# Kernel optimization log

Hardware: AMD Instinct MI355X
Metric: run time of the kernel (lower is better)

Reference implementation:

```python
import jax, jax.numpy as jnp
import numpy as np
import math

D = 768; H = 12; DH = 64; LAT = 512; B = 2; L = 1024


def _rms(x, w, eps=1e-6):
    return w * x * jax.lax.rsqrt(jnp.mean(x * x, axis=-1, keepdims=True) + eps)


def _rope_tables(seq_len, dh):
    inv = 1.0 / (10000.0 ** (np.arange(0, dh, 2, dtype=np.float32) / dh))
    t = np.arange(seq_len, dtype=np.float32)
    f = np.outer(t, inv)
    emb = np.concatenate([f, f], axis=-1)
    return jnp.asarray(np.cos(emb))[None, :, None, :], jnp.asarray(np.sin(emb))[None, :, None, :]


def _rope(x, cos, sin):
    x1, x2 = jnp.split(x, 2, axis=-1)
    return x * cos + jnp.concatenate([-x2, x1], axis=-1) * sin


def setup_inputs():
    key = jax.random.key(0)
    ks = jax.random.split(key, 8)
    s = 0.02
    return {
        'x': jax.random.normal(ks[0], (B, L, D), jnp.float32),
        'w_ln': jnp.ones((D,), jnp.float32),
        'w_compress': jax.random.normal(ks[1], (D, LAT), jnp.float32) * s,
        'w_qkv': jax.random.normal(ks[2], (LAT, 3 * D), jnp.float32) * s,
        'w_reso': jax.random.normal(ks[3], (LAT, H * 4), jnp.float32) * s,
        'w_qn': jnp.ones((DH,), jnp.float32),
        'w_kn': jnp.ones((DH,), jnp.float32),
        'head_decay': jnp.linspace(-3.0, 1.0, H).astype(jnp.float32),
        'temperature': jnp.ones((1,), jnp.float32) * 0.5,
        'w_out_gate': jax.random.normal(ks[4], (LAT, D), jnp.float32) * s,
        'w_proj': jax.random.normal(ks[5], (D, D), jnp.float32) * s,
        'w_memnorm': jnp.ones((D,), jnp.float32),
    }


def reference(x, w_ln, w_compress, w_qkv, w_reso, w_qn, w_kn, head_decay, temperature, w_out_gate, w_proj, w_memnorm):
    cos, sin = _rope_tables(L, DH)
    xn = _rms(x, w_ln)
    latent = jax.nn.silu(xn @ w_compress)                        # (B,L,LAT)
    q, k, v = jnp.split(latent @ w_qkv, 3, axis=-1)
    q = _rope(_rms(q.reshape(B, L, H, DH), w_qn), cos, sin)
    k = _rope(_rms(k.reshape(B, L, H, DH), w_kn), cos, sin)
    v_f = v.reshape(B, L, H, DH)
    q_f = jax.nn.elu(q) + 1.0
    k_f = jax.nn.elu(k) + 1.0
    params = (latent @ w_reso).reshape(B, L, H, 4)
    sem_amp, sem_phase, ctx_amp, ctx_phase = [params[..., i] for i in range(4)]
    sem_phase = jax.nn.sigmoid(sem_phase) * math.pi
    ctx_phase = jax.nn.sigmoid(ctx_phase) * math.pi
    decay = jnp.clip(0.3 + 0.65 * jax.nn.sigmoid(head_decay), 1e-5, 0.999)   # (H,)
    gate = jnp.clip(jax.nn.sigmoid(jax.nn.sigmoid(sem_amp) * jax.nn.sigmoid(ctx_amp)
                                   * jnp.cos(sem_phase - ctx_phase) * temperature[0]) * 1.2 - 0.1,
                    0.05, 0.95)                                  # (B,L,H)
    one_m = (1.0 - decay)[None, None, :]                          # (1,1,H)
    kv_in = jnp.einsum('blhd,blhe->blhde', k_f, v_f) * gate[..., None, None] * one_m[..., None, None]
    z_in = k_f * one_m[..., None]
    # cumulative log-decay -> df, same as torch cumsum of constant per-step log_decay
    cum_log = jnp.arange(1, L + 1, dtype=jnp.float32)[:, None] * jnp.log(decay)[None, :]
    df = jnp.exp(cum_log)[None, :, :, None]                       # (1,L,H,1)
    kv_states = jnp.cumsum(kv_in / (df[..., None] + 1e-8), axis=1) * df[..., None]
    z_states = jnp.cumsum(z_in / (df + 1e-8), axis=1) * df
    out_num = jnp.einsum('blhd,blhde->blhe', q_f, kv_states)
    den = jnp.clip(jnp.sum(q_f * z_states, axis=-1, keepdims=True), 1e-5, None)
    out = (out_num / den).reshape(B, L, D)
    return (_rms(out, w_memnorm) @ w_proj) * jax.nn.silu(latent @ w_out_gate)
```

## Files before the change

kernel.cpp:

```cpp
#include <hip/hip_runtime.h>
#include <hip/hip_bf16.h>
#include <math.h>

#define D_MODEL 768
#define NHEAD   12
#define LATD    512
#define BATCH   2
#define SEQ     1024
#define NROWS   (BATCH*SEQ)
#define NCHUNK  (SEQ/64)
#define NBH     (BATCH*NHEAD)
#define NFUSE   3200
#define PQ      72

using short8 = __attribute__((ext_vector_type(8))) short;
using f32x4  = __attribute__((ext_vector_type(4))) float;

__device__ __forceinline__ float sigf(float x){ return 1.f/(1.f+expf(-x)); }
__device__ __forceinline__ float decay_of(float hd){
  float d = 0.3f + 0.65f*sigf(hd);
  return fminf(fmaxf(d, 1e-5f), 0.999f);
}
__device__ __forceinline__ unsigned short f2b(float f){
  __hip_bfloat16 h = __float2bfloat16(f);
  return *reinterpret_cast<unsigned short*>(&h);
}
__device__ __forceinline__ float bf2f(unsigned short u){
  unsigned int x = ((unsigned int)u) << 16;
  return __uint_as_float(x);
}
__device__ __forceinline__ void async16(const unsigned short* g, unsigned short* l){
  __builtin_amdgcn_global_load_lds((const __attribute__((address_space(1))) void*)g,
                                   (__attribute__((address_space(3))) void*)l, 16, 0, 0);
}

__device__ __forceinline__ void rms_row(const float* __restrict__ xr,
    const float* __restrict__ w, unsigned short* __restrict__ yr,
    int tid, float* red)
{
  float v0 = xr[tid], v1 = xr[tid+256], v2 = xr[tid+512];
  float s = v0*v0 + v1*v1 + v2*v2;
  #pragma unroll
  for (int off=32; off; off>>=1) s += __shfl_xor(s, off, 64);
  if ((tid & 63) == 0) red[tid>>6] = s;
  __syncthreads();
  s = red[0]+red[1]+red[2]+red[3];
  float sc = rsqrtf(s*(1.f/(float)D_MODEL) + 1e-6f);
  yr[tid]     = f2b(v0*sc*w[tid]);
  yr[tid+256] = f2b(v1*sc*w[tid+256]);
  yr[tid+512] = f2b(v2*sc*w[tid+512]);
}

__global__ __launch_bounds__(256) void k_rmsnorm_bf(const float* __restrict__ x,
    const float* __restrict__ w, unsigned short* __restrict__ y)
{
  __shared__ float red[4];
  int row = blockIdx.x, tid = threadIdx.x;
  rms_row(x + (size_t)row*D_MODEL, w, y + (size_t)row*D_MODEL, tid, red);
}

__global__ __launch_bounds__(256) void k_prep(
    const float* __restrict__ x, const float* __restrict__ w_ln,
    unsigned short* __restrict__ xn,
    const float* __restrict__ wc, const float* __restrict__ wq,
    const float* __restrict__ wr, const float* __restrict__ wg,
    const float* __restrict__ wp,
    unsigned short* __restrict__ wtc, unsigned short* __restrict__ wtq,
    unsigned short* __restrict__ wtg, unsigned short* __restrict__ wtp)
{
  __shared__ unsigned short tile[64][65];
  __shared__ float red[4];
  int blk = blockIdx.x, t = threadIdx.x;
  if (blk >= 640){
    int row = blk - 640;
    rms_row(x + (size_t)row*D_MODEL, w_ln, xn + (size_t)row*D_MODEL, t, red);
    return;
  }
  const float* W; unsigned short* WT; int K, N, bx, by;
  if (blk < 96){ W=wc; WT=wtc; K=768; N=512; bx=blk&7; by=blk>>3; }
  else if (blk < 384){ int i=blk-96;  W=wq; WT=wtq; K=512; N=2304; bx=i%36; by=i/36; }
  else if (blk < 480){ int i=blk-384; W=wg; WT=wtg; K=512; N=768;  bx=i%12; by=i/12; }
  else if (blk < 624){ int i=blk-480; W=wp; WT=wtp; K=768; N=768;  bx=i%12; by=i/12; }
  else {
    int i = blk - 624;
    #pragma unroll
    for (int j=0;j<16;j++){
      int e = i*4096 + t + j*256;
      int n = 2304 + (e >> 9), k = e & 511;
      float v = (n < 2352) ? wr[(size_t)k*48 + (n-2304)] : 0.f;
      wtq[(size_t)n*512 + k] = f2b(v);
    }
    return;
  }
  int k0 = by*64, n0 = bx*64, cr = t >> 6, cc = t & 63;
  #pragma unroll
  for (int i=0;i<16;i++){
    int r = cr + i*4;
    tile[r][cc] = f2b(W[(size_t)(k0+r)*N + n0 + cc]);
  }
  __syncthreads();
  #pragma unroll
  for (int i=0;i<16;i++){
    int nn = cr + i*4;
    WT[(size_t)(n0+nn)*K + k0 + cc] = tile[cc][nn];
  }
}

__global__ __launch_bounds__(256) void k_gemm64(const unsigned short* __restrict__ A,
    const unsigned short* __restrict__ BT, float* __restrict__ Cf,
    unsigned short* __restrict__ Cb, const unsigned short* __restrict__ auxb,
    int M, int N, int K, int act, int NX)
{
  __shared__ unsigned short As[2*64*64];
  __shared__ unsigned short Bs[2*64*64];
  int tid = threadIdx.x;
  int w = tid >> 6, lane = tid & 63;
  int m16 = lane & 15, quad = lane >> 4;
  int bid = blockIdx.x, cpx = gridDim.x >> 3;
  int swz = (bid & 7)*cpx + (bid >> 3);
  int bx = swz % NX, by = swz / NX;
  int bm = by*64, bn = bx*64;

  f32x4 acc[4];
  #pragma unroll
  for (int nt=0;nt<4;nt++) acc[nt] = (f32x4){0.f,0.f,0.f,0.f};

  int nk = K >> 6;
  #pragma unroll
  for (int i=0;i<2;i++){
    int g = (w*2 + i)*64 + lane;
    int m = g >> 3, c = (g & 7) ^ (m & 7);
    async16(A  + (size_t)(bm+m)*K + c*8, As + (w*2+i)*512);
    async16(BT + (size_t)(bn+m)*K + c*8, Bs + (w*2+i)*512);
  }
  __syncthreads();
  int cur = 0;
  for (int t = 0; t < nk; ++t){
    if (t+1 < nk){
      int kk = (t+1) << 6;
      int nb = cur ^ 1;
      #pragma unroll
      for (int i=0;i<2;i++){
        int g = (w*2 + i)*64 + lane;
        int m = g >> 3, c = (g & 7) ^ (m & 7);
        async16(A  + (size_t)(bm+m)*K + kk + c*8, As + nb*4096 + (w*2+i)*512);
        async16(BT + (size_t)(bn+m)*K + kk + c*8, Bs + nb*4096 + (w*2+i)*512);
      }
    }
    #pragma unroll
    for (int s=0;s<2;s++){
      int row = w*16 + m16;
      short8 af = *(const short8*)(As + cur*4096 + (row*8 + ((s*4 + quad) ^ (row & 7)))*8);
      #pragma unroll
      for (int nt=0;nt<4;nt++){
        int n = nt*16 + m16;
        short8 bf = *(const short8*)(Bs + cur*4096 + (n*8 + ((s*4 + quad) ^ (n & 7)))*8);
        acc[nt] = __builtin_amdgcn_mfma_f32_16x16x32_bf16(af, bf, acc[nt], 0, 0, 0);
      }
    }
    __syncthreads();
    cur ^= 1;
  }
  #pragma unroll
  for (int r=0;r<4;r++){
    int row = bm + w*16 + quad*4 + r;
    #pragma unroll
    for (int nt=0;nt<4;nt++){
      int col = bn + nt*16 + m16;
      float v = acc[nt][r];
      if (act == 1) v = v/(1.f + __expf(-v));
      else if (act == 2) v *= bf2f(auxb[(size_t)row*N + col]);
      if (Cf) Cf[(size_t)row*N + col] = v;
      if (Cb) Cb[(size_t)row*N + col] = f2b(v);
    }
  }
}

__global__ __launch_bounds__(256) void k_gemm_fused(const unsigned short* __restrict__ A,
    const unsigned short* __restrict__ BT, const float* __restrict__ w_qn,
    const float* __restrict__ w_kn, const float* __restrict__ hdec,
    const float* __restrict__ temp, unsigned short* __restrict__ qf,
    unsigned short* __restrict__ kf, unsigned short* __restrict__ vf,
    float* __restrict__ cKV, float* __restrict__ cG,
    unsigned short* __restrict__ gateb)
{
  __shared__ __align__(16) unsigned short SM[4*128*64];
  unsigned short* As = SM;
  unsigned short* Bs = SM + 2*128*64;
  const int K = LATD;
  int tid = threadIdx.x;
  int w = tid >> 6, lane = tid & 63;
  int wm = (w >> 1)*64, wn = (w & 1)*64;
  int m16 = lane & 15, quad = lane >> 4;
  int bid = blockIdx.x;
  int swz = (bid & 7)*50 + (bid >> 3);
  int bx = swz >> 4, by = swz & 15;
  int bm = by*128, bn = bx*128;

  f32x4 acc[4][4];
  #pragma unroll
  for (int i=0;i<4;i++)
    #pragma unroll
    for (int j=0;j<4;j++) acc[i][j] = (f32x4){0.f,0.f,0.f,0.f};

  const int nk = K >> 6;
  #pragma unroll
  for (int i=0;i<4;i++){
    int g = (w*4 + i)*64 + lane;
    int m = g >> 3, c = (g & 7) ^ (m & 7);
    async16(A  + (size_t)(bm+m)*K + c*8, As + (w*4+i)*512);
    async16(BT + (size_t)(bn+m)*K + c*8, Bs + (w*4+i)*512);
  }
  __syncthreads();
  int cur = 0;
  for (int t = 0; t < nk; ++t){
    if (t+1 < nk){
      int kk = (t+1) << 6;
      int nb = cur ^ 1;
      #pragma unroll
      for (int i=0;i<4;i++){
        int g = (w*4 + i)*64 + lane;
        int m = g >> 3, c = (g & 7) ^ (m & 7);
        async16(A  + (size_t)(bm+m)*K + kk + c*8, As + nb*8192 + (w*4+i)*512);
        async16(BT + (size_t)(bn+m)*K + kk + c*8, Bs + nb*8192 + (w*4+i)*512);
      }
    }
    #pragma unroll
    for (int s=0;s<2;s++){
      short8 af[4], bf[4];
      #pragma unroll
      for (int mt=0;mt<4;mt++){
        int m = wm + mt*16 + m16;
        int idx = m*8 + ((s*4 + quad) ^ (m & 7));
        af[mt] = *(const short8*)(As + cur*8192 + idx*8);
      }
      #pragma unroll
      for (int nt=0;nt<4;nt++){
        int n = wn + nt*16 + m16;
        int idx = n*8 + ((s*4 + quad) ^ (n & 7));
        bf[nt] = *(const short8*)(Bs + cur*8192 + idx*8);
      }
      #pragma unroll
      for (int mt=0;mt<4;mt++)
        #pragma unroll
        for (int nt=0;nt<4;nt++)
          acc[mt][nt] = __builtin_amdgcn_mfma_f32_16x16x32_bf16(af[mt], bf[nt], acc[mt][nt], 0, 0, 0);
    }
    __syncthreads();
    cur ^= 1;
  }

  int colbase = bn + wn;
  if (colbase < 2304){
    int sec = colbase >= 1536 ? 2 : (colbase >= 768 ? 1 : 0);
    int h = (colbase - sec*768) >> 6;
    if (sec == 2){
      #pragma unroll
      for (int mt=0;mt<4;mt++)
        #pragma unroll
        for (int r=0;r<4;r++){
          int row = bm + wm + mt*16 + quad*4 + r;
          int b = row >> 10, t = row & 1023;
          size_t ob = (((size_t)(b*NHEAD+h))*SEQ + t)*64;
          #pragma unroll
          for (int nt=0;nt<4;nt++)
            vf[ob + nt*16 + m16] = f2b(acc[mt][nt][r]);
        }
    } else {
      const float* wnp = sec ? w_kn : w_qn;
      unsigned short* of = sec ? kf : qf;
      float wv4[4];
      #pragma unroll
      for (int nt=0;nt<4;nt++) wv4[nt] = wnp[nt*16 + m16];
      float inv0 = exp2f(-(float)m16*(1.f/32.f)*13.28771237954945f);
      float inv1 = inv0 * 0.01f;
      #pragma unroll
      for (int mt=0;mt<4;mt++)
        #pragma unroll
        for (int r=0;r<4;r++){
          int row = bm + wm + mt*16 + quad*4 + r;
          int b = row >> 10, t = row & 1023;
          float s = 0.f;
          #pragma unroll
          for (int nt=0;nt<4;nt++) s += acc[mt][nt][r]*acc[mt][nt][r];
          s += __shfl_xor(s, 1, 64); s += __shfl_xor(s, 2, 64);
          s += __shfl_xor(s, 4, 64); s += __shfl_xor(s, 8, 64);
          float rs = rsqrtf(s*(1.f/64.f) + 1e-6f);
          float qv[4];
          #pragma unroll
          for (int nt=0;nt<4;nt++) qv[nt] = acc[mt][nt][r]*rs*wv4[nt];
          float s0,c0,s1,c1;
          __sincosf((float)t*inv0, &s0, &c0);
          __sincosf((float)t*inv1, &s1, &c1);
          size_t ob = (((size_t)(b*NHEAD+h))*SEQ + t)*64;
          #pragma unroll
          for (int nt=0;nt<4;nt++){
            float rot = (nt < 2) ? -qv[nt+2] : qv[nt-2];
            float cs = (nt & 1) ? c1 : c0, sn = (nt & 1) ? s1 : s0;
            float val = qv[nt]*cs + rot*sn;
            val = (val > 0.f) ? val + 1.f : __expf(val);
            of[ob + nt*16 + m16] = f2b(val);
          }
        }
    }
  } else if (colbase < 2432){
    float* pf = (float*)SM;
    if (colbase == 2304){
      #pragma unroll
      for (int mt=0;mt<4;mt++)
        #pragma unroll
        for (int r=0;r<4;r++){
          int rowl = wm + mt*16 + quad*4 + r;
          #pragma unroll
          for (int nt=0;nt<4;nt++){
            int p = nt*16 + m16;
            if (p < 48) pf[rowl*49 + p] = acc[mt][nt][r];
          }
        }
    }
    __syncthreads();
    float tv = temp[0];
    #pragma unroll
    for (int i=0;i<6;i++){
      int idx2 = tid + i*256;
      int rowl = idx2 / 12, h = idx2 - rowl*12;
      int row = bm + rowl, b = row >> 10, t = row & 1023;
      const float* pr = pf + rowl*49 + h*4;
      float sa = sigf(pr[0]);
      float sp = sigf(pr[1])*3.14159265358979323846f;
      float ca = sigf(pr[2]);
      float cp = sigf(pr[3])*3.14159265358979323846f;
      float z = sa*ca*cosf(sp - cp)*tv;
      float gate = fminf(fmaxf(sigf(z)*1.2f - 0.1f, 0.05f), 0.95f);
      float dd = decay_of(hdec[h]);
      float df = expf((float)(t+1)*logf(dd));
      float g = df/(df + 1e-8f);
      int ci = (b*NHEAD + h)*SEQ + t;
      cKV[ci] = g*gate*(1.f - dd);
      cG[ci]  = 1.f/gate;
    }
  } else {
    #pragma unroll
    for (int mt=0;mt<4;mt++)
      #pragma unroll
      for (int r=0;r<4;r++){
        int row = bm + wm + mt*16 + quad*4 + r;
        #pragma unroll
        for (int nt=0;nt<4;nt++){
          int gc = colbase + nt*16 + m16 - 2432;
          float v = acc[mt][nt][r];
          v = v/(1.f + __expf(-v));
          gateb[(size_t)row*D_MODEL + gc] = f2b(v);
        }
      }
  }
}

__global__ __launch_bounds__(256) void k_intra(const unsigned short* __restrict__ qf,
    const unsigned short* __restrict__ kf, const unsigned short* __restrict__ vf,
    const float* __restrict__ cKVb, const float* __restrict__ cGb,
    const float* __restrict__ hdec, float* __restrict__ numb,
    float* __restrict__ denb, float* __restrict__ Pb, float* __restrict__ zPb)
{
  __shared__ __align__(16) unsigned short Qb[64*PQ];
  __shared__ __align__(16) unsigned short Kb[64*PQ];
  __shared__ __align__(16) unsigned short KtS[64*PQ];
  __shared__ __align__(16) unsigned short Wb[64*PQ];
  __shared__ __align__(16) unsigned short Vt[80*PQ];
  __shared__ float cn[64], cps[64];
  int bid = blockIdx.x;
  int chunk = bid & 15, bh = bid >> 4, h = bh % NHEAD;
  int tid = threadIdx.x, w = tid >> 6, lane = tid & 63;
  int m16 = lane & 15, quad = lane >> 4;
  size_t base = ((size_t)bh*SEQ + chunk*64)*64;
  float d = decay_of(hdec[h]);
  float l2d = log2f(d);

  if (tid < 64){
    float c = cKVb[bh*SEQ + chunk*64 + tid];
    float pw = exp2f((float)(63 - tid)*l2d);
    cn[tid] = c;
    cps[tid] = c*pw;
    Vt[64*PQ + tid] = f2b(cGb[bh*SEQ + chunk*64 + tid]);
  }
  for (int i = tid; i < 15*PQ; i += 256) Vt[65*PQ + i] = 0;
  __syncthreads();

  #pragma unroll
  for (int i=0;i<2;i++){
    int g = tid + i*256;
    int r = g >> 3, c8 = (g & 7)*8;
    *(short8*)(Qb + r*PQ + c8) = *(const short8*)(qf + base + r*64 + c8);
    *(short8*)(Kb + r*PQ + c8) = *(const short8*)(kf + base + r*64 + c8);
  }
  {
    int s = tid & 63;
    float cpss = cps[s];
    #pragma unroll
    for (int i=0;i<2;i++){
      int c8 = ((tid >> 6) + i*4)*8;
      short8 vv = *(const short8*)(vf + base + s*64 + c8);
      short8 kk = *(const short8*)(kf + base + s*64 + c8);
      #pragma unroll
      for (int j=0;j<8;j++){
        Vt[(c8+j)*PQ + s] = ((unsigned short*)&vv)[j];
        KtS[(c8+j)*PQ + s] = f2b(bf2f(((unsigned short*)&kk)[j])*cpss);
      }
    }
  }
  __syncthreads();

  int trow = w*16 + quad*4;
  for (int stile=0; stile<4; stile++){
    if (stile > w){
      #pragma unroll
      for (int r=0;r<4;r++) Wb[(trow+r)*PQ + stile*16 + m16] = 0;
      continue;
    }
    f32x4 acc = (f32x4){0.f,0.f,0.f,0.f};
    #pragma unroll
    for (int ks=0;ks<2;ks++){
      short8 a = *(const short8*)(Qb + (w*16 + m16)*PQ + ks*32 + quad*8);
      short8 b = *(const short8*)(Kb + (stile*16 + m16)*PQ + ks*32 + quad*8);
      acc = __builtin_amdgcn_mfma_f32_16x16x32_bf16(a, b, acc, 0, 0, 0);
    }
    int s = stile*16 + m16;
    float cns = cn[s];
    #pragma unroll
    for (int r=0;r<4;r++){
      int t = trow + r;
      float wv = 0.f;
      if (s <= t) wv = acc[r]*exp2f((float)(t-s)*l2d)*cns;
      Wb[t*PQ + s] = f2b(wv);
    }
  }
  __syncthreads();

  {
    f32x4 acc[5];
    #pragma unroll
    for (int et=0;et<5;et++) acc[et] = (f32x4){0.f,0.f,0.f,0.f};
    #pragma unroll
    for (int et=0;et<5;et++)
      #pragma unroll
      for (int ks=0;ks<2;ks++){
        short8 a = *(const short8*)(Wb + (w*16 + m16)*PQ + ks*32 + quad*8);
        short8 b = *(const short8*)(Vt + (et*16 + m16)*PQ + ks*32 + quad*8);
        acc[et] = __builtin_amdgcn_mfma_f32_16x16x32_bf16(a, b, acc[et], 0, 0, 0);
      }
    #pragma unroll
    for (int et=0;et<4;et++)
      #pragma unroll
      for (int r=0;r<4;r++)
        numb[base + (size_t)(trow+r)*64 + et*16 + m16] = acc[et][r];
    if (m16 == 0){
      #pragma unroll
      for (int r=0;r<4;r++)
        denb[bh*SEQ + chunk*64 + trow + r] = acc[4][r];
    }
  }
  {
    #pragma unroll
    for (int j=0;j<5;j++){
      int tIdx = w + 4*j;
      int et = tIdx >> 2, dt = tIdx & 3;
      f32x4 acc = (f32x4){0.f,0.f,0.f,0.f};
      #pragma unroll
      for (int ks=0;ks<2;ks++){
        short8 a = *(const short8*)(Vt  + (et*16 + m16)*PQ + ks*32 + quad*8);
        short8 b = *(const short8*)(KtS + (dt*16 + m16)*PQ + ks*32 + quad*8);
        acc = __builtin_amdgcn_mfma_f32_16x16x32_bf16(a, b, acc, 0, 0, 0);
      }
      if (et < 4){
        #pragma unroll
        for (int r=0;r<4;r++)
          Pb[(size_t)bid*4096 + (et*16 + quad*4 + r)*64 + dt*16 + m16] = acc[r];
      } else {
        if (quad == 0) zPb[bid*64 + dt*16 + m16] = acc[0];
      }
    }
  }
}

__global__ __launch_bounds__(256) void k_cross(const unsigned short* __restrict__ qf,
    const float* __restrict__ Pb, const float* __restrict__ zPb,
    const float* __restrict__ numb, const float* __restrict__ denb,
    const float* __restrict__ hdec, float* __restrict__ attn)
{
  __shared__ __align__(16) unsigned short Qb[64*PQ];
  __shared__ __align__(16) unsigned short Sp[80*PQ];
  __shared__ float den_sm[64];
  int bid = blockIdx.x;
  int swz = (bid & 7)*48 + (bid >> 3);
  int chunk = swz & 15, bh = swz >> 4;
  int h = bh % NHEAD, b = bh / NHEAD;
  int tid = threadIdx.x, w = tid >> 6, lane = tid & 63;
  int m16 = lane & 15, quad = lane >> 4;
  size_t base = ((size_t)bh*SEQ + chunk*64)*64;
  float d = decay_of(hdec[h]);
  float l2d = log2f(d);
  float d64l2 = 64.f*l2d;

  #pragma unroll
  for (int i=0;i<2;i++){
    int g = tid + i*256;
    int r = g >> 3, c8 = (g & 7)*8;
    *(short8*)(Qb + r*PQ + c8) = *(const short8*)(qf + base + r*64 + c8);
  }

  {
    int r = tid >> 3, c8 = (tid & 7)*8;
    float a0[8], a1[8];
    #pragma unroll
    for (int j=0;j<8;j++){ a0[j]=0.f; a1[j]=0.f; }
    for (int c=0;c<chunk;c++){
      float wgt = exp2f((float)(chunk-1-c)*d64l2);
      const float* ps = Pb + ((size_t)(bh*NCHUNK + c))*4096;
      float4 p0 = *(const float4*)(ps + r*64 + c8);
      float4 p1 = *(const float4*)(ps + r*64 + c8 + 4);
      float4 p2 = *(const float4*)(ps + (r+32)*64 + c8);
      float4 p3 = *(const float4*)(ps + (r+32)*64 + c8 + 4);
      a0[0]+=wgt*p0.x; a0[1]+=wgt*p0.y; a0[2]+=wgt*p0.z; a0[3]+=wgt*p0.w;
      a0[4]+=wgt*p1.x; a0[5]+=wgt*p1.y; a0[6]+=wgt*p1.z; a0[7]+=wgt*p1.w;
      a1[0]+=wgt*p2.x; a1[1]+=wgt*p2.y; a1[2]+=wgt*p2.z; a1[3]+=wgt*p2.w;
      a1[4]+=wgt*p3.x; a1[5]+=wgt*p3.y; a1[6]+=wgt*p3.z; a1[7]+=wgt*p3.w;
    }
    #pragma unroll
    for (int j=0;j<8;j++){
      Sp[r*PQ + c8 + j]      = f2b(a0[j]);
      Sp[(r+32)*PQ + c8 + j] = f2b(a1[j]);
    }
  }
  if (tid < 64){
    float z = 0.f;
    for (int c=0;c<chunk;c++)
      z += exp2f((float)(chunk-1-c)*d64l2) * zPb[(bh*NCHUNK + c)*64 + tid];
    Sp[64*PQ + tid] = f2b(z);
  }
  for (int i = tid; i < 15*PQ; i += 256) Sp[65*PQ + i] = 0;
  __syncthreads();

  f32x4 acc[5];
  #pragma unroll
  for (int et=0;et<5;et++) acc[et] = (f32x4){0.f,0.f,0.f,0.f};
  #pragma unroll
  for (int et=0;et<5;et++)
    #pragma unroll
    for (int ks=0;ks<2;ks++){
      short8 a = *(const short8*)(Qb + (w*16 + m16)*PQ + ks*32 + quad*8);
      short8 bb = *(const short8*)(Sp + (et*16 + m16)*PQ + ks*32 + quad*8);
      acc[et] = __builtin_amdgcn_mfma_f32_16x16x32_bf16(a, bb, acc[et], 0, 0, 0);
    }
  int trow = w*16 + quad*4;
  if (m16 == 0){
    #pragma unroll
    for (int r=0;r<4;r++){
      int tl = trow + r;
      float pw = exp2f((float)(tl+1)*l2d);
      float den = fmaxf(denb[bh*SEQ + chunk*64 + tl] + pw*acc[4][r], 1e-5f);
      den_sm[tl] = 1.f/den;
    }
  }
  __syncthreads();
  #pragma unroll
  for (int r=0;r<4;r++){
    int tl = trow + r;
    float pw = exp2f((float)(tl+1)*l2d);
    float invden = den_sm[tl];
    int tg = chunk*64 + tl;
    #pragma unroll
    for (int et=0;et<4;et++){
      int e = et*16 + m16;
      float nm = numb[base + (size_t)tl*64 + e] + pw*acc[et][r];
      attn[((size_t)(b*SEQ + tg))*D_MODEL + h*64 + e] = nm*invden;
    }
  }
}

extern "C" void kernel_launch(void* const* d_in, const int* in_sizes, int n_in,
                              void* d_out, int out_size, void* d_ws, size_t ws_size,
                              hipStream_t stream)
{
  (void)in_sizes; (void)n_in; (void)out_size; (void)ws_size;
  const float* x       = (const float*)d_in[0];
  const float* w_ln    = (const float*)d_in[1];
  const float* w_comp  = (const float*)d_in[2];
  const float* w_qkv   = (const float*)d_in[3];
  const float* w_reso  = (const float*)d_in[4];
  const float* w_qn    = (const float*)d_in[5];
  const float* w_kn    = (const float*)d_in[6];
  const float* hdec    = (const float*)d_in[7];
  const float* temp    = (const float*)d_in[8];
  const float* w_ogate = (const float*)d_in[9];
  const float* w_proj  = (const float*)d_in[10];
  const float* w_mn    = (const float*)d_in[11];
  float* ws = (float*)d_ws;
  float* out = (float*)d_out;

  const size_t o_cKV    = 0;
  const size_t o_cG     = o_cKV    + (size_t)NBH*SEQ;
  const size_t o_den    = o_cG     + (size_t)NBH*SEQ;
  const size_t o_P      = o_den    + (size_t)NBH*SEQ;
  const size_t o_zP     = o_P      + (size_t)NBH*NCHUNK*4096;
  const size_t o_attn   = o_zP     + (size_t)NBH*NCHUNK*64;
  const size_t o_numb   = o_attn   + (size_t)NROWS*D_MODEL;
  const size_t o_end    = o_numb   + (size_t)NBH*SEQ*64;

  unsigned short* bws = (unsigned short*)(ws + o_end);
  const size_t u_xn     = 0;
  const size_t u_latent = u_xn     + (size_t)NROWS*D_MODEL;
  const size_t u_memn   = u_latent + (size_t)NROWS*LATD;
  const size_t u_q      = u_memn   + (size_t)NROWS*D_MODEL;
  const size_t u_k      = u_q      + (size_t)NBH*SEQ*64;
  const size_t u_v      = u_k      + (size_t)NBH*SEQ*64;
  const size_t u_gate   = u_v      + (size_t)NBH*SEQ*64;
  const size_t u_wtc    = u_gate   + (size_t)NROWS*D_MODEL;
  const size_t u_wtq    = u_wtc    + (size_t)LATD*D_MODEL;
  const size_t u_wtg    = u_wtq    + (size_t)2432*LATD;
  const size_t u_wtp    = u_wtg    + (size_t)D_MODEL*LATD;

  k_prep<<<2688, 256, 0, stream>>>(x, w_ln, bws + u_xn,
      w_comp, w_qkv, w_reso, w_ogate, w_proj,
      bws + u_wtc, bws + u_wtq, bws + u_wtg, bws + u_wtp);
  k_gemm64<<<256, 256, 0, stream>>>(bws + u_xn, bws + u_wtc,
      nullptr, bws + u_latent, nullptr, NROWS, LATD, D_MODEL, 1, LATD/64);
  k_gemm_fused<<<400, 256, 0, stream>>>(bws + u_latent, bws + u_wtq,
      w_qn, w_kn, hdec, temp, bws + u_q, bws + u_k, bws + u_v,
      ws + o_cKV, ws + o_cG, bws + u_gate);
  k_intra<<<NBH*NCHUNK, 256, 0, stream>>>(bws + u_q, bws + u_k, bws + u_v,
      ws + o_cKV, ws + o_cG, hdec, ws + o_numb, ws + o_den, ws + o_P, ws + o_zP);
  k_cross<<<NBH*NCHUNK, 256, 0, stream>>>(bws + u_q, ws + o_P, ws + o_zP,
      ws + o_numb, ws + o_den, hdec, ws + o_attn);
  k_rmsnorm_bf<<<NROWS, 256, 0, stream>>>(ws + o_attn, w_mn, bws + u_memn);
  k_gemm64<<<384, 256, 0, stream>>>(bws + u_memn, bws + u_wtp,
      out, nullptr, bws + u_gate, NROWS, D_MODEL, D_MODEL, 2, D_MODEL/64);
}
```

Measured before the change: 150.3 us.

## Fuse memory RMSNorm into cross kernel and output GEMM epilogue

Removes the standalone RMSNorm kernel over the attention output. The cross kernel now writes the attention output directly as bf16 and atomically accumulates per-row sums of squares. The norm weight is folded into the transposed projection weights during prep, and the final GEMM epilogue applies the per-row rsqrt scale. This saves one launch and an fp32 round trip of the attention tensor, at the cost of atomics and bf16 rounding before normalization.

```diff
diff --git a/kernel.cpp b/kernel.cpp
--- a/kernel.cpp
+++ b/kernel.cpp
@@ -51,22 +51,15 @@
   yr[tid+512] = f2b(v2*sc*w[tid+512]);
 }
 
-__global__ __launch_bounds__(256) void k_rmsnorm_bf(const float* __restrict__ x,
-    const float* __restrict__ w, unsigned short* __restrict__ y)
-{
-  __shared__ float red[4];
-  int row = blockIdx.x, tid = threadIdx.x;
-  rms_row(x + (size_t)row*D_MODEL, w, y + (size_t)row*D_MODEL, tid, red);
-}
-
 __global__ __launch_bounds__(256) void k_prep(
     const float* __restrict__ x, const float* __restrict__ w_ln,
     unsigned short* __restrict__ xn,
     const float* __restrict__ wc, const float* __restrict__ wq,
     const float* __restrict__ wr, const float* __restrict__ wg,
-    const float* __restrict__ wp,
+    const float* __restrict__ wp, const float* __restrict__ w_mn,
     unsigned short* __restrict__ wtc, unsigned short* __restrict__ wtq,
-    unsigned short* __restrict__ wtg, unsigned short* __restrict__ wtp)
+    unsigned short* __restrict__ wtg, unsigned short* __restrict__ wtp,
+    float* __restrict__ sumsq)
 {
   __shared__ unsigned short tile[64][65];
   __shared__ float red[4];
@@ -77,12 +70,17 @@
     return;
   }
   const float* W; unsigned short* WT; int K, N, bx, by;
+  const float* kscale = nullptr;
   if (blk < 96){ W=wc; WT=wtc; K=768; N=512; bx=blk&7; by=blk>>3; }
   else if (blk < 384){ int i=blk-96;  W=wq; WT=wtq; K=512; N=2304; bx=i%36; by=i/36; }
   else if (blk < 480){ int i=blk-384; W=wg; WT=wtg; K=512; N=768;  bx=i%12; by=i/12; }
-  else if (blk < 624){ int i=blk-480; W=wp; WT=wtp; K=768; N=768;  bx=i%12; by=i/12; }
+  else if (blk < 624){ int i=blk-480; W=wp; WT=wtp; K=768; N=768;  bx=i%12; by=i/12; kscale=w_mn; }
   else {
     int i = blk - 624;
+    if (i == 0){
+      #pragma unroll
+      for (int j=0;j<8;j++) sumsq[t + j*256] = 0.f;
+    }
     #pragma unroll
     for (int j=0;j<16;j++){
       int e = i*4096 + t + j*256;
@@ -96,7 +94,9 @@
   #pragma unroll
   for (int i=0;i<16;i++){
     int r = cr + i*4;
-    tile[r][cc] = f2b(W[(size_t)(k0+r)*N + n0 + cc]);
+    float v = W[(size_t)(k0+r)*N + n0 + cc];
+    if (kscale) v *= kscale[k0+r];
+    tile[r][cc] = f2b(v);
   }
   __syncthreads();
   #pragma unroll
@@ -109,7 +109,7 @@
 __global__ __launch_bounds__(256) void k_gemm64(const unsigned short* __restrict__ A,
     const unsigned short* __restrict__ BT, float* __restrict__ Cf,
     unsigned short* __restrict__ Cb, const unsigned short* __restrict__ auxb,
-    int M, int N, int K, int act, int NX)
+    const float* __restrict__ sums, int M, int N, int K, int act, int NX)
 {
   __shared__ unsigned short As[2*64*64];
   __shared__ unsigned short Bs[2*64*64];
@@ -164,12 +164,14 @@
   #pragma unroll
   for (int r=0;r<4;r++){
     int row = bm + w*16 + quad*4 + r;
+    float rowsc = 1.f;
+    if (act == 3) rowsc = rsqrtf(sums[row]*(1.f/(float)D_MODEL) + 1e-6f);
     #pragma unroll
     for (int nt=0;nt<4;nt++){
       int col = bn + nt*16 + m16;
       float v = acc[nt][r];
       if (act == 1) v = v/(1.f + __expf(-v));
-      else if (act == 2) v *= bf2f(auxb[(size_t)row*N + col]);
+      else if (act == 3) v = v*rowsc*bf2f(auxb[(size_t)row*N + col]);
       if (Cf) Cf[(size_t)row*N + col] = v;
       if (Cb) Cb[(size_t)row*N + col] = f2b(v);
     }
@@ -485,7 +487,8 @@
 __global__ __launch_bounds__(256) void k_cross(const unsigned short* __restrict__ qf,
     const float* __restrict__ Pb, const float* __restrict__ zPb,
     const float* __restrict__ numb, const float* __restrict__ denb,
-    const float* __restrict__ hdec, float* __restrict__ attn)
+    const float* __restrict__ hdec, unsigned short* __restrict__ attnb,
+    float* __restrict__ sumsq)
 {
   __shared__ __align__(16) unsigned short Qb[64*PQ];
   __shared__ __align__(16) unsigned short Sp[80*PQ];
@@ -567,13 +570,18 @@
     int tl = trow + r;
     float pw = exp2f((float)(tl+1)*l2d);
     float invden = den_sm[tl];
-    int tg = chunk*64 + tl;
+    int rowg = b*SEQ + chunk*64 + tl;
+    float ls = 0.f;
     #pragma unroll
     for (int et=0;et<4;et++){
       int e = et*16 + m16;
-      float nm = numb[base + (size_t)tl*64 + e] + pw*acc[et][r];
-      attn[((size_t)(b*SEQ + tg))*D_MODEL + h*64 + e] = nm*invden;
-    }
+      float ov = (numb[base + (size_t)tl*64 + e] + pw*acc[et][r])*invden;
+      attnb[(size_t)rowg*D_MODEL + h*64 + e] = f2b(ov);
+      ls += ov*ov;
+    }
+    ls += __shfl_xor(ls, 1, 64); ls += __shfl_xor(ls, 2, 64);
+    ls += __shfl_xor(ls, 4, 64); ls += __shfl_xor(ls, 8, 64);
+    if (m16 == 0) atomicAdd(&sumsq[rowg], ls);
   }
 }
 
@@ -602,8 +610,8 @@
   const size_t o_den    = o_cG     + (size_t)NBH*SEQ;
   const size_t o_P      = o_den    + (size_t)NBH*SEQ;
   const size_t o_zP     = o_P      + (size_t)NBH*NCHUNK*4096;
-  const size_t o_attn   = o_zP     + (size_t)NBH*NCHUNK*64;
-  const size_t o_numb   = o_attn   + (size_t)NROWS*D_MODEL;
+  const size_t o_sumsq  = o_zP     + (size_t)NBH*NCHUNK*64;
+  const size_t o_numb   = o_sumsq  + (size_t)NROWS;
   const size_t o_end    = o_numb   + (size_t)NBH*SEQ*64;
 
   unsigned short* bws = (unsigned short*)(ws + o_end);
@@ -620,18 +628,17 @@
   const size_t u_wtp    = u_wtg    + (size_t)D_MODEL*LATD;
 
   k_prep<<<2688, 256, 0, stream>>>(x, w_ln, bws + u_xn,
-      w_comp, w_qkv, w_reso, w_ogate, w_proj,
-      bws + u_wtc, bws + u_wtq, bws + u_wtg, bws + u_wtp);
+      w_comp, w_qkv, w_reso, w_ogate, w_proj, w_mn,
+      bws + u_wtc, bws + u_wtq, bws + u_wtg, bws + u_wtp, ws + o_sumsq);
   k_gemm64<<<256, 256, 0, stream>>>(bws + u_xn, bws + u_wtc,
-      nullptr, bws + u_latent, nullptr, NROWS, LATD, D_MODEL, 1, LATD/64);
+      nullptr, bws + u_latent, nullptr, nullptr, NROWS, LATD, D_MODEL, 1, LATD/64);
   k_gemm_fused<<<400, 256, 0, stream>>>(bws + u_latent, bws + u_wtq,
       w_qn, w_kn, hdec, temp, bws + u_q, bws + u_k, bws + u_v,
       ws + o_cKV, ws + o_cG, bws + u_gate);
   k_intra<<<NBH*NCHUNK, 256, 0, stream>>>(bws + u_q, bws + u_k, bws + u_v,
       ws + o_cKV, ws + o_cG, hdec, ws + o_numb, ws + o_den, ws + o_P, ws + o_zP);
   k_cross<<<NBH*NCHUNK, 256, 0, stream>>>(bws + u_q, ws + o_P, ws + o_zP,
-      ws + o_numb, ws + o_den, hdec, ws + o_attn);
-  k_rmsnorm_bf<<<NROWS, 256, 0, stream>>>(ws + o_attn, w_mn, bws + u_memn);
+      ws + o_numb, ws + o_den, hdec, bws + u_memn, ws + o_sumsq);
   k_gemm64<<<384, 256, 0, stream>>>(bws + u_memn, bws + u_wtp,
-      out, nullptr, bws + u_gate, NROWS, D_MODEL, D_MODEL, 2, D_MODEL/64);
-}
+      out, nullptr, bws + u_gate, ws + o_sumsq, NROWS, D_MODEL, D_MODEL, 3, D_MODEL/64);
+}
```

Result: no change. 150.2 us (median of 2 runs) (-0.1%).
